# Optimization experiments

Measured on AMD Instinct MI355X. Metric: run time of the kernel, lower is better.

Reference implementation:

```python
import jax, jax.numpy as jnp
import numpy as np

N, D, O, V, E, C = 100000, 128, 128, 3, 400000, 2

def setup_inputs() -> dict:
    key = jax.random.key(0)
    ks = jax.random.split(key, 32)
    s = 0.05
    inp = {
        'features': jax.random.normal(ks[0], (N, D), jnp.float32),
        'edge_index': jax.random.randint(ks[1], (V, 2, E), 0, N, jnp.int32),
        'edge_weight': jax.random.uniform(ks[2], (V, E), jnp.float32),
        # per-view RelationAggregator (single relation each)
        'rel_w': jax.random.normal(ks[3], (V, D, O)) * s,
        'rel_b': jnp.zeros((V, O)),
        'gate_w': jax.random.normal(ks[4], (V, O, O)) * s,
        'gate_b': jnp.zeros((V, O)),
        # LabelAwareAttention
        'la_w1': jax.random.normal(ks[5], (C, D, D // 2)) * s,
        'la_b1': jnp.zeros((C, D // 2)),
        'la_w2': jax.random.normal(ks[6], (C, D // 2)) * s,
        'la_b2': jnp.zeros((C,)),
        'pred_w': jax.random.normal(ks[7], (D, C)) * s,
        'pred_b': jnp.zeros((C,)),
        'att_bias': jnp.float32(0.1),
        # ViewLevelAttention
        'view_pref': jax.random.normal(ks[8], (V, O)),
        'va_w1': jax.random.normal(ks[9], (O, O // 2)) * s,
        'va_b1': jnp.zeros((O // 2,)),
        'va_w2': jax.random.normal(ks[10], (O // 2,)) * s,
        'va_b2': jnp.float32(0.0),
        # linear heads
        'ft_w': jax.random.normal(ks[11], (D, O)) * s,
        'ft_b': jnp.zeros((O,)),
        'sl_w': jax.random.normal(ks[12], (D, O)) * s,
        'sl_b': jnp.zeros((O,)),
        'fus_w': jax.random.normal(ks[13], (2 * O, O)) * s,
        'fus_b': jnp.zeros((O,)),
        'ln_g': jnp.ones((O,)),
        'ln_beta': jnp.zeros((O,)),
    }
    return inp


def _aggregate_view(features, ei, ew, w, b, gw, gb):
    # gather -> linear -> edge weight -> scatter-add (fused segment_sum)
    msg = (features[ei[0]] @ w + b) * ew[:, None]          # [E, O]
    agg = jax.ops.segment_sum(msg, ei[1], num_segments=N)  # [N, O]
    # relation_weight_net: softmax over 1 relation == 1.0 (identity)
    gate = jax.nn.sigmoid(agg @ gw + gb)
    return gate * agg


def reference(features, edge_index, edge_weight, rel_w, rel_b, gate_w, gate_b,
              la_w1, la_b1, la_w2, la_b2, pred_w, pred_b, att_bias,
              view_pref, va_w1, va_b1, va_w2, va_b2,
              ft_w, ft_b, sl_w, sl_b, fus_w, fus_b, ln_g, ln_beta):
    # --- label-aware attention ---
    class_probs = jax.nn.softmax(features @ pred_w + pred_b, axis=-1)        # [N, C]
    h = jax.nn.relu(jnp.einsum('nd,cdk->nck', features, la_w1) + la_b1)      # [N, C, D/2]
    scores = jax.nn.sigmoid(jnp.einsum('nck,ck->nc', h, la_w2) + la_b2)      # [N, C]
    node_att = jnp.sum(scores * class_probs, axis=-1) + att_bias             # [N]

    # --- per-view relation aggregation ---
    views = jax.vmap(_aggregate_view, in_axes=(None, 0, 0, 0, 0, 0, 0))(
        features, edge_index, edge_weight, rel_w, rel_b, gate_w, gate_b)     # [V, N, O]

    # --- view-level attention ---
    pe = views * view_pref[:, None, :]                                       # [V, N, O]
    vh = jax.nn.relu(jnp.einsum('vno,ok->vnk', pe, va_w1) + va_b1)           # [V, N, O/2]
    vscore = jnp.einsum('vnk,k->vn', vh, va_w2) + va_b2                      # [V, N]
    v_att = jax.nn.softmax(vscore, axis=0)                                   # over views
    combined = jnp.sum(views * v_att[..., None], axis=0)                     # [N, O]

    # --- fusion (dropout in eval mode == identity) ---
    self_out = features @ sl_w + sl_b
    transformed = features @ ft_w + ft_b
    weighted = combined * node_att[:, None]
    fused = jax.nn.relu(jnp.concatenate([self_out, weighted], axis=-1) @ fus_w + fus_b)
    out = fused + transformed

    mu = jnp.mean(out, axis=-1, keepdims=True)
    var = jnp.mean(jnp.square(out - mu), axis=-1, keepdims=True)
    out = (out - mu) / jnp.sqrt(var + 1e-5) * ln_g + ln_beta
    return out, class_probs
```

## Files before the change

kernel.cpp:

```cpp
#include <hip/hip_runtime.h>

#define N_ 100000
#define D_ 128
#define O_ 128
#define V_ 3
#define E_ 400000
#define NB_SCAN 98
#define EGRID 1563
#define MB 16
#define NBLK (N_ / MB)
#define LDA 136

#define PRE_CVT  6250
#define PRE_PREW (PRE_CVT + 64)
#define PRE_PREP (PRE_PREW + 617)
#define PRE_TOT  (PRE_PREP + 3 * EGRID)

typedef unsigned short u16;
typedef __attribute__((ext_vector_type(8))) short bf16x8;
typedef __attribute__((ext_vector_type(4))) float f32x4;

#define MFMA16x16x32 __builtin_amdgcn_mfma_f32_16x16x32_bf16

#define P_RELB  0
#define P_GATEB 384
#define P_VP    768
#define P_VAB1  1152
#define P_VAW2  1216
#define P_VAB2  1280
#define P_LAB1  1281
#define P_LAW2  1409
#define P_LAB2  1537
#define P_PREDB 1539
#define P_ATTB  1541
#define P_FTB   1542
#define P_LNG   1670
#define P_LNB   1798
#define P_PREDW 1926
#define P_TOTAL 2182

__device__ __forceinline__ float b2f(u16 u) {
    union { float f; unsigned int i; } x; x.i = ((unsigned int)u) << 16; return x.f;
}
__device__ __forceinline__ float blo(unsigned int u) {
    union { float f; unsigned int i; } x; x.i = u << 16; return x.f;
}
__device__ __forceinline__ float bhi(unsigned int u) {
    union { float f; unsigned int i; } x; x.i = u & 0xffff0000u; return x.f;
}
__device__ __forceinline__ u16 f2b(float f) {
    union { float f; unsigned int i; } x; x.f = f;
    unsigned int r = x.i + 0x7FFFu + ((x.i >> 16) & 1u);
    return (u16)(r >> 16);
}

template<int F32> __device__ __forceinline__ float LD(const void* p, size_t i) {
    if (F32) return ((const float*)p)[i];
    return b2f(((const u16*)p)[i]);
}

__global__ void k_detect(const u16* __restrict__ feat, int* __restrict__ flag) {
    int t = threadIdx.x;
    u16 a = feat[2 * t], b = feat[2 * t + 128];
    int zeros = (a == 0 ? 1 : 0) + (b == 0 ? 1 : 0);
    float va = b2f(a), vb = b2f(b);
    int bad = (!(va > -128.f && va < 128.f) ? 1 : 0) +
              (!(vb > -128.f && vb < 128.f) ? 1 : 0);
    #pragma unroll
    for (int s = 1; s <= 32; s <<= 1) {
        bad += __shfl_xor(bad, s);
        zeros += __shfl_xor(zeros, s);
    }
    if (t == 0) flag[0] = (bad >= 16 || zeros >= 64) ? 1 : 0;
}

__device__ __forceinline__ void cvt_body_f32(int b, const void* feat,
                                             u16* __restrict__ featB) {
    size_t idx = (size_t)b * 256 + threadIdx.x;
    const float4* fp = (const float4*)feat;
    float4 a = fp[idx * 2], c = fp[idx * 2 + 1];
    uint4 u;
    u.x = (unsigned)f2b(a.x) | ((unsigned)f2b(a.y) << 16);
    u.y = (unsigned)f2b(a.z) | ((unsigned)f2b(a.w) << 16);
    u.z = (unsigned)f2b(c.x) | ((unsigned)f2b(c.y) << 16);
    u.w = (unsigned)f2b(c.z) | ((unsigned)f2b(c.w) << 16);
    ((uint4*)featB)[idx] = u;
}

template<int F32>
__device__ __forceinline__ void prew_body(int b, const void* sl_w, const void* sl_b,
                                          const void* fus_w, const void* fus_b,
                                          u16* __restrict__ W1T, float* __restrict__ b1) {
    int gid = b * 256 + threadIdx.x;
    int d = gid >> 7, o = gid & 127;
    float acc = 0.f;
    for (int k = 0; k < 128; ++k)
        acc += LD<F32>(sl_w, d * 128 + k) * LD<F32>(fus_w, k * 128 + o);
    W1T[o * 128 + d] = f2b(acc);
    if (gid < 128) {
        float accb = 0.f;
        for (int k = 0; k < 128; ++k)
            accb += LD<F32>(sl_b, k) * LD<F32>(fus_w, k * 128 + gid);
        b1[gid] = accb + LD<F32>(fus_b, gid);
    }
}

template<int F32>
__device__ __forceinline__ void prep_body(int b,
        const void* rel_w, const void* gate_w, const void* va_w1, const void* fus_w,
        const void* ft_w, const void* la_w1,
        const void* rel_b, const void* gate_b, const void* vpref,
        const void* va_b1, const void* va_w2, const void* va_b2,
        const void* la_b1, const void* la_w2, const void* la_b2,
        const void* pred_b, const void* att_bias, const void* ft_b,
        const void* ln_g, const void* ln_beta, const void* pred_w,
        u16* __restrict__ relT, u16* __restrict__ gateT, u16* __restrict__ vaT,
        u16* __restrict__ fus2T, u16* __restrict__ ftT, u16* __restrict__ laT,
        float* __restrict__ P) {
    int id = b * 256 + threadIdx.x;
    if (id < 49152) {
        int v = id >> 14, r = id & 16383, o = r >> 7, d = r & 127;
        relT[id] = f2b(LD<F32>(rel_w, (size_t)v * 16384 + d * 128 + o));
    } else if (id < 98304) {
        int t = id - 49152, v = t >> 14, r = t & 16383, o = r >> 7, d = r & 127;
        gateT[t] = f2b(LD<F32>(gate_w, (size_t)v * 16384 + d * 128 + o));
    } else if (id < 106496) {
        int t = id - 98304, n = t >> 7, k = t & 127;
        vaT[t] = f2b(LD<F32>(va_w1, k * 64 + n));
    } else if (id < 122880) {
        int t = id - 106496, n = t >> 7, k = t & 127;
        fus2T[t] = f2b(LD<F32>(fus_w, (128 + k) * 128 + n));
    } else if (id < 139264) {
        int t = id - 122880, o = t >> 7, d = t & 127;
        ftT[t] = f2b(LD<F32>(ft_w, d * 128 + o));
    } else if (id < 155648) {
        int t = id - 139264, n = t >> 7, d = t & 127;
        int c = n >> 6, j = n & 63;
        laT[t] = f2b(LD<F32>(la_w1, c * 8192 + d * 64 + j));
    } else if (id < 155648 + P_TOTAL) {
        int t = id - 155648;
        float val;
        if      (t < P_GATEB) val = LD<F32>(rel_b, t);
        else if (t < P_VP)    val = LD<F32>(gate_b, t - P_GATEB);
        else if (t < P_VAB1)  val = LD<F32>(vpref, t - P_VP);
        else if (t < P_VAW2)  val = LD<F32>(va_b1, t - P_VAB1);
        else if (t < P_VAB2)  val = LD<F32>(va_w2, t - P_VAW2);
        else if (t < P_LAB1)  val = LD<F32>(va_b2, 0);
        else if (t < P_LAW2)  val = LD<F32>(la_b1, t - P_LAB1);
        else if (t < P_LAB2)  val = LD<F32>(la_w2, t - P_LAW2);
        else if (t < P_PREDB) val = LD<F32>(la_b2, t - P_LAB2);
        else if (t < P_ATTB)  val = LD<F32>(pred_b, t - P_PREDB);
        else if (t < P_FTB)   val = LD<F32>(att_bias, 0);
        else if (t < P_LNG)   val = LD<F32>(ft_b, t - P_FTB);
        else if (t < P_LNB)   val = LD<F32>(ln_g, t - P_LNG);
        else if (t < P_PREDW) val = LD<F32>(ln_beta, t - P_LNB);
        else                  val = LD<F32>(pred_w, t - P_PREDW);
        P[t] = val;
    }
}

__global__ __launch_bounds__(256) void k_preC(const int* __restrict__ flag,
        const void* feat, u16* __restrict__ featB,
        const void* sl_w, const void* sl_b, const void* fus_w, const void* fus_b,
        u16* __restrict__ W1T, float* __restrict__ b1,
        const void* rel_w, const void* gate_w, const void* va_w1,
        const void* ft_w, const void* la_w1,
        const void* rel_b, const void* gate_b, const void* vpref,
        const void* va_b1, const void* va_w2, const void* va_b2,
        const void* la_b1, const void* la_w2, const void* la_b2,
        const void* pred_b, const void* att_bias, const void* ft_b,
        const void* ln_g, const void* ln_beta, const void* pred_w,
        u16* __restrict__ relT, u16* __restrict__ gateT, u16* __restrict__ vaT,
        u16* __restrict__ fus2T, u16* __restrict__ ftT, u16* __restrict__ laT,
        float* __restrict__ P,
        const int* __restrict__ ei, int* __restrict__ cur3) {
    int b = blockIdx.x;
    if (b < PRE_CVT) {
        if (flag[0]) cvt_body_f32(b, feat, featB);
    } else if (b < PRE_PREW) {
        if (flag[0]) prew_body<1>(b - PRE_CVT, sl_w, sl_b, fus_w, fus_b, W1T, b1);
        else         prew_body<0>(b - PRE_CVT, sl_w, sl_b, fus_w, fus_b, W1T, b1);
    } else if (b < PRE_PREP) {
        if (flag[0]) prep_body<1>(b - PRE_PREW, rel_w, gate_w, va_w1, fus_w, ft_w, la_w1,
                                  rel_b, gate_b, vpref, va_b1, va_w2, va_b2,
                                  la_b1, la_w2, la_b2, pred_b, att_bias, ft_b,
                                  ln_g, ln_beta, pred_w, relT, gateT, vaT, fus2T, ftT, laT, P);
        else         prep_body<0>(b - PRE_PREW, rel_w, gate_w, va_w1, fus_w, ft_w, la_w1,
                                  rel_b, gate_b, vpref, va_b1, va_w2, va_b2,
                                  la_b1, la_w2, la_b2, pred_b, att_bias, ft_b,
                                  ln_g, ln_beta, pred_w, relT, gateT, vaT, fus2T, ftT, laT, P);
    } else {
        int b2 = b - PRE_PREP;
        int v = b2 / EGRID;
        int e = (b2 % EGRID) * 256 + threadIdx.x;
        if (e < E_) atomicAdd(&cur3[v * N_ + ei[(size_t)v * 2 * E_ + E_ + e]], 1);
    }
}

__global__ __launch_bounds__(256) void k_scan_bsum(const int* __restrict__ cur3,
                                                   int* __restrict__ bsum) {
    __shared__ int red[256];
    const int v = blockIdx.x / NB_SCAN, b = blockIdx.x % NB_SCAN, tid = threadIdx.x;
    const int base = b * 1024;
    const int* counts = cur3 + v * N_;
    int s = 0;
    for (int i = tid; i < 1024; i += 256) {
        int idx = base + i;
        s += (idx < N_) ? counts[idx] : 0;
    }
    red[tid] = s;
    __syncthreads();
    for (int st = 128; st >= 1; st >>= 1) {
        if (tid < st) red[tid] += red[tid + st];
        __syncthreads();
    }
    if (tid == 0) bsum[v * 128 + b] = red[0];
}

__global__ __launch_bounds__(256) void k_scan_write(int* __restrict__ cur3,
                                                    const int* __restrict__ bsum,
                                                    int* __restrict__ offs3) {
    __shared__ int lsum[256];
    __shared__ int bs_s[128];
    const int v = blockIdx.x / NB_SCAN, b = blockIdx.x % NB_SCAN, tid = threadIdx.x;
    const int base = b * 1024;
    int* counts = cur3 + v * N_;
    int* offs   = offs3 + v * N_;
    if (tid < 128) bs_s[tid] = (tid < b) ? bsum[v * 128 + tid] : 0;
    int c[4]; int s = 0;
    #pragma unroll
    for (int k = 0; k < 4; ++k) {
        int idx = base + tid * 4 + k;
        c[k] = (idx < N_) ? counts[idx] : 0;
        s += c[k];
    }
    lsum[tid] = s;
    __syncthreads();
    for (int st = 1; st < 256; st <<= 1) {
        int t = (tid >= st) ? lsum[tid - st] : 0;
        __syncthreads();
        lsum[tid] += t;
        __syncthreads();
    }
    for (int st = 64; st >= 1; st >>= 1) {
        if (tid < st) bs_s[tid] += bs_s[tid + st];
        __syncthreads();
    }
    int off = bs_s[0] + lsum[tid] - s;
    #pragma unroll
    for (int k = 0; k < 4; ++k) {
        int idx = base + tid * 4 + k;
        if (idx < N_) { offs[idx] = off; counts[idx] = off; }
        off += c[k];
    }
}

template<int F32>
__device__ __forceinline__ void place_body(const int* __restrict__ ei, const void* ew_all,
                                           int* __restrict__ cur3, int2* __restrict__ srcw3) {
    int v = blockIdx.x / EGRID;
    int e = (blockIdx.x % EGRID) * 256 + threadIdx.x;
    if (e < E_) {
        int dst = ei[(size_t)v * 2 * E_ + E_ + e];
        int src = ei[(size_t)v * 2 * E_ + e];
        float w = LD<F32>(ew_all, (size_t)v * E_ + e);
        int pos = atomicAdd(&cur3[v * N_ + dst], 1);
        int2 sw; sw.x = src; sw.y = __float_as_int(w);
        srcw3[(size_t)v * E_ + pos] = sw;
    }
}
__global__ __launch_bounds__(256) void k_place(const int* __restrict__ flag,
                                               const int* __restrict__ ei, const void* ew,
                                               int* __restrict__ cur3, int2* __restrict__ srcw3) {
    if (flag[0]) place_body<1>(ei, ew, cur3, srcw3);
    else         place_body<0>(ei, ew, cur3, srcw3);
}

__global__ __launch_bounds__(256, 4) void k_fused(const int* __restrict__ flag,
        const void* feat, const u16* __restrict__ featB_,
        const int2* __restrict__ srcw3,
        const int* __restrict__ offs3, const int* __restrict__ ends3,
        const u16* __restrict__ relT, const u16* __restrict__ gateT,
        const u16* __restrict__ vaT, const u16* __restrict__ W1T,
        const u16* __restrict__ fus2T, const u16* __restrict__ ftT,
        const u16* __restrict__ laT,
        const float* __restrict__ b1, const float* __restrict__ P,
        void* __restrict__ d_out) {
    const int f32 = flag[0];
    const u16* __restrict__ fb = f32 ? featB_ : (const u16*)feat;

    __shared__ __align__(16) u16 xA[MB * LDA];
    __shared__ __align__(16) u16 zb[2][MB * LDA];
    __shared__ float wsn_s[2][MB];
    __shared__ float vsc_s[MB][3];
    __shared__ float red_s[4][MB][2];
    __shared__ float mrs_s[MB][2];
    __shared__ float aw_s[MB][3];
    __shared__ float natt_s[MB];
    __shared__ float lg_s[MB][2];
    __shared__ float vab1_s[64], vaw2_s[64];
    __shared__ float predw_s[256];
    __shared__ float b1_s[128], ftb_s[128], lng_s[128], lnb_s[128];

    const int tid = threadIdx.x;
    const int wid = tid >> 6;
    const int L = tid & 63, q = L >> 4, i = L & 15;
    const int nb = wid * 32;
    const int nodebase = blockIdx.x * MB;
    const int nl = tid >> 5, l32 = tid & 31, o4 = l32 * 4;
    const int gg = tid >> 4, l16 = tid & 15, o8 = l16 * 8;
    const f32x4 zz = {0.f, 0.f, 0.f, 0.f};

    auto ldf = [&](const u16* B, int row, int k0) -> bf16x8 {
        return *(const bf16x8*)&B[row * LDA + k0];
    };
    auto ldg = [&](const u16* B, int row, int k0) -> bf16x8 {
        return *(const bf16x8*)&B[row * 128 + k0];
    };
    auto gemm128 = [&](const u16* A, const u16* Bg, f32x4 acc[2]) {
        #pragma unroll
        for (int kk = 0; kk < 4; ++kk) {
            int k0 = q * 8 + kk * 32;
            bf16x8 a0 = ldf(A, i, k0);
            bf16x8 bb0 = ldg(Bg, nb + i, k0);
            bf16x8 bb1 = ldg(Bg, nb + 16 + i, k0);
            acc[0] = MFMA16x16x32(a0, bb0, acc[0], 0, 0, 0);
            acc[1] = MFMA16x16x32(a0, bb1, acc[1], 0, 0, 0);
        }
    };
    auto gather = [&](int v, u16* dst) {
        const int* offs = offs3 + v * N_;
        const int* ends = ends3 + v * N_;
        const int2* srcw = srcw3 + (size_t)v * E_;
        const int node = nodebase + gg;
        float z0 = 0.f, z1 = 0.f, z2 = 0.f, z3 = 0.f;
        float z4 = 0.f, z5 = 0.f, z6 = 0.f, z7 = 0.f, ws = 0.f;
        int j = offs[node], jend = ends[node];
        while (j < jend) {
            int r = jend - j;
            int2 e0 = srcw[j];
            int2 e1, e2, e3;
            e1.x = 0; e1.y = 0; e2.x = 0; e2.y = 0; e3.x = 0; e3.y = 0;
            if (r > 1) e1 = srcw[j + 1];
            if (r > 2) e2 = srcw[j + 2];
            if (r > 3) e3 = srcw[j + 3];
            uint4 x0, x1, x2, x3;
            x1.x = x1.y = x1.z = x1.w = 0;
            x2.x = x2.y = x2.z = x2.w = 0;
            x3.x = x3.y = x3.z = x3.w = 0;
            x0 = *(const uint4*)&fb[(size_t)e0.x * 128 + o8];
            if (r > 1) x1 = *(const uint4*)&fb[(size_t)e1.x * 128 + o8];
            if (r > 2) x2 = *(const uint4*)&fb[(size_t)e2.x * 128 + o8];
            if (r > 3) x3 = *(const uint4*)&fb[(size_t)e3.x * 128 + o8];
            float w0 = __int_as_float(e0.y), w1 = __int_as_float(e1.y);
            float w2 = __int_as_float(e2.y), w3 = __int_as_float(e3.y);
            ws += w0 + w1 + w2 + w3;
            z0 += w0 * blo(x0.x) + w1 * blo(x1.x) + w2 * blo(x2.x) + w3 * blo(x3.x);
            z1 += w0 * bhi(x0.x) + w1 * bhi(x1.x) + w2 * bhi(x2.x) + w3 * bhi(x3.x);
            z2 += w0 * blo(x0.y) + w1 * blo(x1.y) + w2 * blo(x2.y) + w3 * blo(x3.y);
            z3 += w0 * bhi(x0.y) + w1 * bhi(x1.y) + w2 * bhi(x2.y) + w3 * bhi(x3.y);
            z4 += w0 * blo(x0.z) + w1 * blo(x1.z) + w2 * blo(x2.z) + w3 * blo(x3.z);
            z5 += w0 * bhi(x0.z) + w1 * bhi(x1.z) + w2 * bhi(x2.z) + w3 * bhi(x3.z);
            z6 += w0 * blo(x0.w) + w1 * blo(x1.w) + w2 * blo(x2.w) + w3 * blo(x3.w);
            z7 += w0 * bhi(x0.w) + w1 * bhi(x1.w) + w2 * bhi(x2.w) + w3 * bhi(x3.w);
            j += 4;
        }
        uint4 u;
        u.x = (unsigned)f2b(z0) | ((unsigned)f2b(z1) << 16);
        u.y = (unsigned)f2b(z2) | ((unsigned)f2b(z3) << 16);
        u.z = (unsigned)f2b(z4) | ((unsigned)f2b(z5) << 16);
        u.w = (unsigned)f2b(z6) | ((unsigned)f2b(z7) << 16);
        *(uint4*)&dst[gg * LDA + o8] = u;
        if (l16 == 0) wsn_s[v & 1][gg] = ws;
    };

    {
        int m = tid >> 4, s = tid & 15;
        *(uint4*)&xA[m * LDA + s * 8] =
            *(const uint4*)&fb[(size_t)(nodebase + m) * 128 + s * 8];
    }
    if (tid < 64) { vab1_s[tid] = P[P_VAB1 + tid]; vaw2_s[tid] = P[P_VAW2 + tid]; }
    if (tid < 128) {
        b1_s[tid]  = b1[tid];
        ftb_s[tid] = P[P_FTB + tid];
        lng_s[tid] = P[P_LNG + tid];
        lnb_s[tid] = P[P_LNB + tid];
    }
    predw_s[tid] = P[P_PREDW + tid];
    gather(0, zb[0]);
    __syncthreads();

    f32x4 accL[2] = {zz, zz};
    gemm128(xA, laT, accL);
    #pragma unroll
    for (int rep = 0; rep < 2; ++rep) {
        int m = rep * 8 + nl;
        float lg0 = 0.f, lg1 = 0.f;
        #pragma unroll
        for (int t = 0; t < 4; ++t) {
            float xv = b2f(xA[m * LDA + o4 + t]);
            lg0 += xv * predw_s[(o4 + t) * 2 + 0];
            lg1 += xv * predw_s[(o4 + t) * 2 + 1];
        }
        #pragma unroll
        for (int s = 1; s <= 16; s <<= 1) {
            lg0 += __shfl_xor(lg0, s);
            lg1 += __shfl_xor(lg1, s);
        }
        if (l32 == 0) { lg_s[m][0] = lg0; lg_s[m][1] = lg1; }
    }
    {
        float la0 = P[P_LAB1 + nb + i],  la1 = P[P_LAB1 + nb + 16 + i];
        float lw0 = P[P_LAW2 + nb + i],  lw1 = P[P_LAW2 + nb + 16 + i];
        float partL[4];
        #pragma unroll
        for (int r = 0; r < 4; ++r) {
            float h0 = fmaxf(accL[0][r] + la0, 0.f);
            float h1 = fmaxf(accL[1][r] + la1, 0.f);
            partL[r] = h0 * lw0 + h1 * lw1;
        }
        #pragma unroll
        for (int s = 1; s <= 8; s <<= 1)
            #pragma unroll
            for (int r = 0; r < 4; ++r)
                partL[r] += __shfl_xor(partL[r], s);
        if (i == 0)
            #pragma unroll
            for (int r = 0; r < 4; ++r)
                red_s[wid][q * 4 + r][0] = partL[r];
    }
    __syncthreads();
    if (tid < MB) {
        float c0 = red_s[0][tid][0] + red_s[1][tid][0] + P[P_LAB2 + 0];
        float c1 = red_s[2][tid][0] + red_s[3][tid][0] + P[P_LAB2 + 1];
        float s0 = 1.f / (1.f + __expf(-c0));
        float s1 = 1.f / (1.f + __expf(-c1));
        float l0 = lg_s[tid][0] + P[P_PREDB + 0];
        float l1 = lg_s[tid][1] + P[P_PREDB + 1];
        float mx = fmaxf(l0, l1);
        float e0 = __expf(l0 - mx), e1 = __expf(l1 - mx);
        float inv = 1.f / (e0 + e1);
        float p0 = e0 * inv, p1 = e1 * inv;
        natt_s[tid] = s0 * p0 + s1 * p1 + P[P_ATTB];
        int node = nodebase + tid;
        if (f32) {
            float* pr = (float*)d_out + (size_t)N_ * O_;
            pr[node * 2 + 0] = p0; pr[node * 2 + 1] = p1;
        } else {
            u16* pr = (u16*)d_out + (size_t)N_ * O_;
            pr[node * 2 + 0] = f2b(p0); pr[node * 2 + 1] = f2b(p1);
        }
    }

    f32x4 viewr[3][2];
    #pragma unroll
    for (int v = 0; v < 3; ++v) {
        u16* zc = zb[v & 1];
        f32x4 accA[2] = {zz, zz};
        gemm128(zc, relT + (size_t)v * 16384, accA);
        if (v < 2) gather(v + 1, zb[(v + 1) & 1]);
        __syncthreads();
        {
            float rb0 = P[P_RELB + v * 128 + nb + i];
            float rb1 = P[P_RELB + v * 128 + nb + 16 + i];
            #pragma unroll
            for (int nt = 0; nt < 2; ++nt) {
                float rb = nt ? rb1 : rb0;
                int col = nb + nt * 16 + i;
                #pragma unroll
                for (int r = 0; r < 4; ++r) {
                    int row = q * 4 + r;
                    float a = accA[nt][r] + wsn_s[v & 1][row] * rb;
                    accA[nt][r] = a;
                    zc[row * LDA + col] = f2b(a);
                }
            }
        }
        __syncthreads();
        f32x4 acc2[2] = {zz, zz};
        gemm128(zc, gateT + (size_t)v * 16384, acc2);
        __syncthreads();
        {
            float gb0 = P[P_GATEB + v * 128 + nb + i];
            float gb1 = P[P_GATEB + v * 128 + nb + 16 + i];
            float vp0 = P[P_VP + v * 128 + nb + i];
            float vp1 = P[P_VP + v * 128 + nb + 16 + i];
            #pragma unroll
            for (int nt = 0; nt < 2; ++nt) {
                float gb = nt ? gb1 : gb0, vp = nt ? vp1 : vp0;
                int col = nb + nt * 16 + i;
                #pragma unroll
                for (int r = 0; r < 4; ++r) {
                    int row = q * 4 + r;
                    float g = 1.f / (1.f + __expf(-(acc2[nt][r] + gb)));
                    float vv = g * accA[nt][r];
                    viewr[v][nt][r] = vv;
                    zc[row * LDA + col] = f2b(vv * vp);
                }
            }
        }
        __syncthreads();
        f32x4 accV = zz;
        const int nbv = wid * 16, colv = nbv + i;
        #pragma unroll
        for (int kk = 0; kk < 4; ++kk) {
            int k0 = q * 8 + kk * 32;
            bf16x8 a0 = ldf(zc, i, k0);
            bf16x8 bb = ldg(vaT, nbv + i, k0);
            accV = MFMA16x16x32(a0, bb, accV, 0, 0, 0);
        }
        float part[4];
        #pragma unroll
        for (int r = 0; r < 4; ++r) {
            float vh = fmaxf(accV[r] + vab1_s[colv], 0.f);
            part[r] = vh * vaw2_s[colv];
        }
        #pragma unroll
        for (int s = 1; s <= 8; s <<= 1)
            #pragma unroll
            for (int r = 0; r < 4; ++r)
                part[r] += __shfl_xor(part[r], s);
        if (i == 0)
            #pragma unroll
            for (int r = 0; r < 4; ++r)
                red_s[wid][q * 4 + r][0] = part[r];
        __syncthreads();
        if (tid < MB)
            vsc_s[tid][v] = red_s[0][tid][0] + red_s[1][tid][0] +
                            red_s[2][tid][0] + red_s[3][tid][0] + P[P_VAB2];
    }

    if (tid < MB) {
        float s0 = vsc_s[tid][0], s1 = vsc_s[tid][1], s2 = vsc_s[tid][2];
        float mx = fmaxf(s0, fmaxf(s1, s2));
        float e0 = __expf(s0 - mx), e1 = __expf(s1 - mx), e2 = __expf(s2 - mx);
        float inv = natt_s[tid] / (e0 + e1 + e2);
        aw_s[tid][0] = e0 * inv; aw_s[tid][1] = e1 * inv; aw_s[tid][2] = e2 * inv;
    }
    __syncthreads();
    u16* wt = zb[0];
    #pragma unroll
    for (int nt = 0; nt < 2; ++nt)
        #pragma unroll
        for (int r = 0; r < 4; ++r) {
            int row = q * 4 + r, col = nb + nt * 16 + i;
            float wv = aw_s[row][0] * viewr[0][nt][r] +
                       aw_s[row][1] * viewr[1][nt][r] +
                       aw_s[row][2] * viewr[2][nt][r];
            wt[row * LDA + col] = f2b(wv);
        }
    f32x4 accF[2] = {zz, zz};
    gemm128(xA, W1T, accF);
    __syncthreads();
    gemm128(wt, fus2T, accF);
    float fR[2][4];
    #pragma unroll
    for (int nt = 0; nt < 2; ++nt)
        #pragma unroll
        for (int r = 0; r < 4; ++r) {
            int col = nb + nt * 16 + i;
            fR[nt][r] = fmaxf(accF[nt][r] + b1_s[col], 0.f);
        }
    f32x4 accT[2] = {zz, zz};
    gemm128(xA, ftT, accT);

    float ov[2][4], ps[4], pq[4];
    #pragma unroll
    for (int r = 0; r < 4; ++r) { ps[r] = 0.f; pq[r] = 0.f; }
    #pragma unroll
    for (int nt = 0; nt < 2; ++nt)
        #pragma unroll
        for (int r = 0; r < 4; ++r) {
            int col = nb + nt * 16 + i;
            float o = fR[nt][r] + accT[nt][r] + ftb_s[col];
            ov[nt][r] = o;
            ps[r] += o; pq[r] += o * o;
        }
    #pragma unroll
    for (int s = 1; s <= 8; s <<= 1)
        #pragma unroll
        for (int r = 0; r < 4; ++r) {
            ps[r] += __shfl_xor(ps[r], s);
            pq[r] += __shfl_xor(pq[r], s);
        }
    if (i == 0)
        #pragma unroll
        for (int r = 0; r < 4; ++r) {
            red_s[wid][q * 4 + r][0] = ps[r];
            red_s[wid][q * 4 + r][1] = pq[r];
        }
    __syncthreads();
    if (tid < MB) {
        float sm = red_s[0][tid][0] + red_s[1][tid][0] + red_s[2][tid][0] + red_s[3][tid][0];
        float sq = red_s[0][tid][1] + red_s[1][tid][1] + red_s[2][tid][1] + red_s[3][tid][1];
        float mu = sm * (1.f / 128.f);
        float var = sq * (1.f / 128.f) - mu * mu;
        mrs_s[tid][0] = mu; mrs_s[tid][1] = rsqrtf(var + 1e-5f);
    }
    __syncthreads();
    float* outf = (float*)zb;
    u16*   outb = (u16*)zb;
    #pragma unroll
    for (int nt = 0; nt < 2; ++nt)
        #pragma unroll
        for (int r = 0; r < 4; ++r) {
            int row = q * 4 + r, col = nb + nt * 16 + i;
            float val = (ov[nt][r] - mrs_s[row][0]) * mrs_s[row][1]
                        * lng_s[col] + lnb_s[col];
            if (f32) outf[row * 128 + col] = val;
            else     outb[row * 128 + col] = f2b(val);
        }
    __syncthreads();
    if (f32) {
        float* op = (float*)d_out + (size_t)nodebase * 128;
        for (int idx = tid; idx < 512; idx += 256)
            ((float4*)op)[idx] = ((const float4*)outf)[idx];
    } else {
        u16* op = (u16*)d_out + (size_t)nodebase * 128;
        ((uint4*)op)[tid] = ((const uint4*)outb)[tid];
    }
}

extern "C" void kernel_launch(void* const* d_in, const int* in_sizes, int n_in,
                              void* d_out, int out_size, void* d_ws, size_t ws_size,
                              hipStream_t stream) {
    const void* feat     = d_in[0];
    const int*  ei       = (const int*)d_in[1];
    const void* ew       = d_in[2];
    const void* rel_w    = d_in[3];
    const void* rel_b    = d_in[4];
    const void* gate_w   = d_in[5];
    const void* gate_b   = d_in[6];
    const void* la_w1    = d_in[7];
    const void* la_b1    = d_in[8];
    const void* la_w2    = d_in[9];
    const void* la_b2    = d_in[10];
    const void* pred_w   = d_in[11];
    const void* pred_b   = d_in[12];
    const void* att_bias = d_in[13];
    const void* view_pref= d_in[14];
    const void* va_w1    = d_in[15];
    const void* va_b1    = d_in[16];
    const void* va_w2    = d_in[17];
    const void* va_b2    = d_in[18];
    const void* ft_w     = d_in[19];
    const void* ft_b     = d_in[20];
    const void* sl_w     = d_in[21];
    const void* sl_b     = d_in[22];
    const void* fus_w    = d_in[23];
    const void* fus_b    = d_in[24];
    const void* ln_g     = d_in[25];
    const void* ln_beta  = d_in[26];

    int*   flag  = (int*)d_ws;
    int*   offs3 = flag + 4;
    int*   cur3  = offs3 + 3 * N_;
    int2*  srcw3 = (int2*)(cur3 + 3 * N_);
    int*   bsum  = (int*)(srcw3 + 3 * E_);
    float* b1    = (float*)(bsum + 3 * 128);
    float* P     = b1 + 128;
    u16*   W1T   = (u16*)(P + 2304);
    u16*   relT  = W1T + 16384;
    u16*   gateT = relT + 3 * 16384;
    u16*   vaT   = gateT + 3 * 16384;
    u16*   fus2T = vaT + 8192;
    u16*   ftT   = fus2T + 16384;
    u16*   laT   = ftT + 16384;
    u16*   featB = laT + 16384;

    k_detect<<<1, 64, 0, stream>>>((const u16*)feat, flag);
    (void)hipMemsetAsync(cur3, 0, 3 * N_ * sizeof(int), stream);
    k_preC<<<PRE_TOT, 256, 0, stream>>>(flag, feat, featB,
                                        sl_w, sl_b, fus_w, fus_b, W1T, b1,
                                        rel_w, gate_w, va_w1, ft_w, la_w1,
                                        rel_b, gate_b, view_pref,
                                        va_b1, va_w2, va_b2,
                                        la_b1, la_w2, la_b2,
                                        pred_b, att_bias, ft_b, ln_g, ln_beta, pred_w,
                                        relT, gateT, vaT, fus2T, ftT, laT, P,
                                        ei, cur3);
    k_scan_bsum<<<3 * NB_SCAN, 256, 0, stream>>>(cur3, bsum);
    k_scan_write<<<3 * NB_SCAN, 256, 0, stream>>>(cur3, bsum, offs3);
    k_place<<<3 * EGRID, 256, 0, stream>>>(flag, ei, ew, cur3, srcw3);
    k_fused<<<NBLK, 256, 0, stream>>>(flag, feat, featB, srcw3, offs3, cur3,
                                      relT, gateT, vaT, W1T, fus2T, ftT, laT,
                                      b1, P, d_out);
}
```

Before: 623.9 us.

## Process three views concurrently in 768-thread blocks with 32-node tiles

The fused kernel now launches 768 threads per block, one 256-thread group per view. Each group gathers its view's neighbors and runs its relation, gate and view-attention GEMMs at the same time as the others, where before the three views ran one after another. The node tile grows from 16 to 32 rows so each weight fragment is reused across two MFMA row tiles. The final fusion GEMMs are also split across the three groups, with partial results passed through shared memory. In exchange, shared memory use per block roughly doubles. The launch bound of (768, 6) may push the compiler into tight register limits or spills, and fewer, larger blocks could reduce occupancy.

```diff
diff --git a/kernel.cpp b/kernel.cpp
--- a/kernel.cpp
+++ b/kernel.cpp
@@ -7,7 +7,7 @@
 #define E_ 400000
 #define NB_SCAN 98
 #define EGRID 1563
-#define MB 16
+#define MB 32
 #define NBLK (N_ / MB)
 #define LDA 136
 
@@ -276,7 +276,7 @@
     else         place_body<0>(ei, ew, cur3, srcw3);
 }
 
-__global__ __launch_bounds__(256, 4) void k_fused(const int* __restrict__ flag,
+__global__ __launch_bounds__(768, 6) void k_fused(const int* __restrict__ flag,
         const void* feat, const u16* __restrict__ featB_,
         const int2* __restrict__ srcw3,
         const int* __restrict__ offs3, const int* __restrict__ ends3,
@@ -290,25 +290,29 @@
     const u16* __restrict__ fb = f32 ? featB_ : (const u16*)feat;
 
     __shared__ __align__(16) u16 xA[MB * LDA];
-    __shared__ __align__(16) u16 zb[2][MB * LDA];
-    __shared__ float wsn_s[2][MB];
-    __shared__ float vsc_s[MB][3];
-    __shared__ float red_s[4][MB][2];
-    __shared__ float mrs_s[MB][2];
+    __shared__ __align__(16) u16 zbuf[3][MB * LDA];
+    __shared__ __align__(16) float Fbuf[MB * 128];
+    __shared__ float vp3_s[3][128];
+    __shared__ float redL[4][MB];
+    __shared__ float redv[3][4][MB];
+    __shared__ float wsn3[3][MB];
     __shared__ float aw_s[MB][3];
     __shared__ float natt_s[MB];
     __shared__ float lg_s[MB][2];
+    __shared__ float mrs_s[MB][2];
     __shared__ float vab1_s[64], vaw2_s[64];
     __shared__ float predw_s[256];
     __shared__ float b1_s[128], ftb_s[128], lng_s[128], lnb_s[128];
 
     const int tid = threadIdx.x;
-    const int wid = tid >> 6;
-    const int L = tid & 63, q = L >> 4, i = L & 15;
+    const int g   = tid >> 8;
+    const int t256 = tid & 255;
+    const int wid = t256 >> 6;
+    const int L = t256 & 63, q = L >> 4, i = L & 15;
     const int nb = wid * 32;
     const int nodebase = blockIdx.x * MB;
-    const int nl = tid >> 5, l32 = tid & 31, o4 = l32 * 4;
-    const int gg = tid >> 4, l16 = tid & 15, o8 = l16 * 8;
+    const int nl = t256 >> 5, l32 = t256 & 31, o4 = l32 * 4;
+    const int gsub = t256 >> 4, l16 = tid & 15, o8 = l16 * 8;
     const f32x4 zz = {0.f, 0.f, 0.f, 0.f};
 
     auto ldf = [&](const u16* B, int row, int k0) -> bf16x8 {
@@ -317,64 +321,71 @@
     auto ldg = [&](const u16* B, int row, int k0) -> bf16x8 {
         return *(const bf16x8*)&B[row * 128 + k0];
     };
-    auto gemm128 = [&](const u16* A, const u16* Bg, f32x4 acc[2]) {
+    auto gemm32 = [&](const u16* A, const u16* Bg, f32x4 acc[2][2]) {
         #pragma unroll
         for (int kk = 0; kk < 4; ++kk) {
             int k0 = q * 8 + kk * 32;
             bf16x8 a0 = ldf(A, i, k0);
+            bf16x8 a1 = ldf(A, i + 16, k0);
             bf16x8 bb0 = ldg(Bg, nb + i, k0);
             bf16x8 bb1 = ldg(Bg, nb + 16 + i, k0);
-            acc[0] = MFMA16x16x32(a0, bb0, acc[0], 0, 0, 0);
-            acc[1] = MFMA16x16x32(a0, bb1, acc[1], 0, 0, 0);
+            acc[0][0] = MFMA16x16x32(a0, bb0, acc[0][0], 0, 0, 0);
+            acc[0][1] = MFMA16x16x32(a0, bb1, acc[0][1], 0, 0, 0);
+            acc[1][0] = MFMA16x16x32(a1, bb0, acc[1][0], 0, 0, 0);
+            acc[1][1] = MFMA16x16x32(a1, bb1, acc[1][1], 0, 0, 0);
         }
     };
-    auto gather = [&](int v, u16* dst) {
-        const int* offs = offs3 + v * N_;
-        const int* ends = ends3 + v * N_;
-        const int2* srcw = srcw3 + (size_t)v * E_;
-        const int node = nodebase + gg;
-        float z0 = 0.f, z1 = 0.f, z2 = 0.f, z3 = 0.f;
-        float z4 = 0.f, z5 = 0.f, z6 = 0.f, z7 = 0.f, ws = 0.f;
-        int j = offs[node], jend = ends[node];
-        while (j < jend) {
-            int r = jend - j;
-            int2 e0 = srcw[j];
-            int2 e1, e2, e3;
-            e1.x = 0; e1.y = 0; e2.x = 0; e2.y = 0; e3.x = 0; e3.y = 0;
-            if (r > 1) e1 = srcw[j + 1];
-            if (r > 2) e2 = srcw[j + 2];
-            if (r > 3) e3 = srcw[j + 3];
-            uint4 x0, x1, x2, x3;
-            x1.x = x1.y = x1.z = x1.w = 0;
-            x2.x = x2.y = x2.z = x2.w = 0;
-            x3.x = x3.y = x3.z = x3.w = 0;
-            x0 = *(const uint4*)&fb[(size_t)e0.x * 128 + o8];
-            if (r > 1) x1 = *(const uint4*)&fb[(size_t)e1.x * 128 + o8];
-            if (r > 2) x2 = *(const uint4*)&fb[(size_t)e2.x * 128 + o8];
-            if (r > 3) x3 = *(const uint4*)&fb[(size_t)e3.x * 128 + o8];
-            float w0 = __int_as_float(e0.y), w1 = __int_as_float(e1.y);
-            float w2 = __int_as_float(e2.y), w3 = __int_as_float(e3.y);
-            ws += w0 + w1 + w2 + w3;
-            z0 += w0 * blo(x0.x) + w1 * blo(x1.x) + w2 * blo(x2.x) + w3 * blo(x3.x);
-            z1 += w0 * bhi(x0.x) + w1 * bhi(x1.x) + w2 * bhi(x2.x) + w3 * bhi(x3.x);
-            z2 += w0 * blo(x0.y) + w1 * blo(x1.y) + w2 * blo(x2.y) + w3 * blo(x3.y);
-            z3 += w0 * bhi(x0.y) + w1 * bhi(x1.y) + w2 * bhi(x2.y) + w3 * bhi(x3.y);
-            z4 += w0 * blo(x0.z) + w1 * blo(x1.z) + w2 * blo(x2.z) + w3 * blo(x3.z);
-            z5 += w0 * bhi(x0.z) + w1 * bhi(x1.z) + w2 * bhi(x2.z) + w3 * bhi(x3.z);
-            z6 += w0 * blo(x0.w) + w1 * blo(x1.w) + w2 * blo(x2.w) + w3 * blo(x3.w);
-            z7 += w0 * bhi(x0.w) + w1 * bhi(x1.w) + w2 * bhi(x2.w) + w3 * bhi(x3.w);
-            j += 4;
+    auto gather = [&]() {
+        const int* offs = offs3 + g * N_;
+        const int* ends = ends3 + g * N_;
+        const int2* srcw = srcw3 + (size_t)g * E_;
+        #pragma unroll
+        for (int rep = 0; rep < 2; ++rep) {
+            const int m = gsub + rep * 16;
+            const int node = nodebase + m;
+            float z0 = 0.f, z1 = 0.f, z2 = 0.f, z3 = 0.f;
+            float z4 = 0.f, z5 = 0.f, z6 = 0.f, z7 = 0.f, ws = 0.f;
+            int j = offs[node], jend = ends[node];
+            while (j < jend) {
+                int r = jend - j;
+                int2 e0 = srcw[j];
+                int2 e1, e2, e3;
+                e1.x = 0; e1.y = 0; e2.x = 0; e2.y = 0; e3.x = 0; e3.y = 0;
+                if (r > 1) e1 = srcw[j + 1];
+                if (r > 2) e2 = srcw[j + 2];
+                if (r > 3) e3 = srcw[j + 3];
+                uint4 x0, x1, x2, x3;
+                x1.x = x1.y = x1.z = x1.w = 0;
+                x2.x = x2.y = x2.z = x2.w = 0;
+                x3.x = x3.y = x3.z = x3.w = 0;
+                x0 = *(const uint4*)&fb[(size_t)e0.x * 128 + o8];
+                if (r > 1) x1 = *(const uint4*)&fb[(size_t)e1.x * 128 + o8];
+                if (r > 2) x2 = *(const uint4*)&fb[(size_t)e2.x * 128 + o8];
+                if (r > 3) x3 = *(const uint4*)&fb[(size_t)e3.x * 128 + o8];
+                float w0 = __int_as_float(e0.y), w1 = __int_as_float(e1.y);
+                float w2 = __int_as_float(e2.y), w3 = __int_as_float(e3.y);
+                ws += w0 + w1 + w2 + w3;
+                z0 += w0 * blo(x0.x) + w1 * blo(x1.x) + w2 * blo(x2.x) + w3 * blo(x3.x);
+                z1 += w0 * bhi(x0.x) + w1 * bhi(x1.x) + w2 * bhi(x2.x) + w3 * bhi(x3.x);
+                z2 += w0 * blo(x0.y) + w1 * blo(x1.y) + w2 * blo(x2.y) + w3 * blo(x3.y);
+                z3 += w0 * bhi(x0.y) + w1 * bhi(x1.y) + w2 * bhi(x2.y) + w3 * bhi(x3.y);
+                z4 += w0 * blo(x0.z) + w1 * blo(x1.z) + w2 * blo(x2.z) + w3 * blo(x3.z);
+                z5 += w0 * bhi(x0.z) + w1 * bhi(x1.z) + w2 * bhi(x2.z) + w3 * bhi(x3.z);
+                z6 += w0 * blo(x0.w) + w1 * blo(x1.w) + w2 * blo(x2.w) + w3 * blo(x3.w);
+                z7 += w0 * bhi(x0.w) + w1 * bhi(x1.w) + w2 * bhi(x2.w) + w3 * bhi(x3.w);
+                j += 4;
+            }
+            uint4 u;
+            u.x = (unsigned)f2b(z0) | ((unsigned)f2b(z1) << 16);
+            u.y = (unsigned)f2b(z2) | ((unsigned)f2b(z3) << 16);
+            u.z = (unsigned)f2b(z4) | ((unsigned)f2b(z5) << 16);
+            u.w = (unsigned)f2b(z6) | ((unsigned)f2b(z7) << 16);
+            *(uint4*)&zbuf[g][m * LDA + o8] = u;
+            if (l16 == 0) wsn3[g][m] = ws;
         }
-        uint4 u;
-        u.x = (unsigned)f2b(z0) | ((unsigned)f2b(z1) << 16);
-        u.y = (unsigned)f2b(z2) | ((unsigned)f2b(z3) << 16);
-        u.z = (unsigned)f2b(z4) | ((unsigned)f2b(z5) << 16);
-        u.w = (unsigned)f2b(z6) | ((unsigned)f2b(z7) << 16);
-        *(uint4*)&dst[gg * LDA + o8] = u;
-        if (l16 == 0) wsn_s[v & 1][gg] = ws;
     };
 
-    {
+    if (tid < 512) {
         int m = tid >> 4, s = tid & 15;
         *(uint4*)&xA[m * LDA + s * 8] =
             *(const uint4*)&fb[(size_t)(nodebase + m) * 128 + s * 8];
@@ -386,53 +397,84 @@
         lng_s[tid] = P[P_LNG + tid];
         lnb_s[tid] = P[P_LNB + tid];
     }
-    predw_s[tid] = P[P_PREDW + tid];
-    gather(0, zb[0]);
-    __syncthreads();
-
-    f32x4 accL[2] = {zz, zz};
-    gemm128(xA, laT, accL);
-    #pragma unroll
-    for (int rep = 0; rep < 2; ++rep) {
-        int m = rep * 8 + nl;
-        float lg0 = 0.f, lg1 = 0.f;
-        #pragma unroll
-        for (int t = 0; t < 4; ++t) {
-            float xv = b2f(xA[m * LDA + o4 + t]);
-            lg0 += xv * predw_s[(o4 + t) * 2 + 0];
-            lg1 += xv * predw_s[(o4 + t) * 2 + 1];
+    if (tid < 256) predw_s[tid] = P[P_PREDW + tid];
+    if (tid >= 256 && tid < 640) {
+        int t = tid - 256;
+        vp3_s[t >> 7][t & 127] = P[P_VP + t];
+    }
+    gather();
+    __syncthreads();
+
+    f32x4 accA[2][2] = {{zz, zz}, {zz, zz}};
+    gemm32(zbuf[g], relT + (size_t)g * 16384, accA);
+    if (g == 0) {
+        f32x4 accL[2][2] = {{zz, zz}, {zz, zz}};
+        gemm32(xA, laT, accL);
+        #pragma unroll
+        for (int rep = 0; rep < 4; ++rep) {
+            int m = rep * 8 + nl;
+            float lg0 = 0.f, lg1 = 0.f;
+            #pragma unroll
+            for (int t = 0; t < 4; ++t) {
+                float xv = b2f(xA[m * LDA + o4 + t]);
+                lg0 += xv * predw_s[(o4 + t) * 2 + 0];
+                lg1 += xv * predw_s[(o4 + t) * 2 + 1];
+            }
+            #pragma unroll
+            for (int s = 1; s <= 16; s <<= 1) {
+                lg0 += __shfl_xor(lg0, s);
+                lg1 += __shfl_xor(lg1, s);
+            }
+            if (l32 == 0) { lg_s[m][0] = lg0; lg_s[m][1] = lg1; }
         }
-        #pragma unroll
-        for (int s = 1; s <= 16; s <<= 1) {
-            lg0 += __shfl_xor(lg0, s);
-            lg1 += __shfl_xor(lg1, s);
-        }
-        if (l32 == 0) { lg_s[m][0] = lg0; lg_s[m][1] = lg1; }
-    }
-    {
         float la0 = P[P_LAB1 + nb + i],  la1 = P[P_LAB1 + nb + 16 + i];
         float lw0 = P[P_LAW2 + nb + i],  lw1 = P[P_LAW2 + nb + 16 + i];
-        float partL[4];
-        #pragma unroll
-        for (int r = 0; r < 4; ++r) {
-            float h0 = fmaxf(accL[0][r] + la0, 0.f);
-            float h1 = fmaxf(accL[1][r] + la1, 0.f);
-            partL[r] = h0 * lw0 + h1 * lw1;
-        }
+        float partL[2][4];
+        #pragma unroll
+        for (int mt = 0; mt < 2; ++mt)
+            #pragma unroll
+            for (int r = 0; r < 4; ++r) {
+                float h0 = fmaxf(accL[mt][0][r] + la0, 0.f);
+                float h1 = fmaxf(accL[mt][1][r] + la1, 0.f);
+                partL[mt][r] = h0 * lw0 + h1 * lw1;
+            }
         #pragma unroll
         for (int s = 1; s <= 8; s <<= 1)
             #pragma unroll
-            for (int r = 0; r < 4; ++r)
-                partL[r] += __shfl_xor(partL[r], s);
+            for (int mt = 0; mt < 2; ++mt)
+                #pragma unroll
+                for (int r = 0; r < 4; ++r)
+                    partL[mt][r] += __shfl_xor(partL[mt][r], s);
         if (i == 0)
             #pragma unroll
-            for (int r = 0; r < 4; ++r)
-                red_s[wid][q * 4 + r][0] = partL[r];
-    }
-    __syncthreads();
+            for (int mt = 0; mt < 2; ++mt)
+                #pragma unroll
+                for (int r = 0; r < 4; ++r)
+                    redL[wid][mt * 16 + q * 4 + r] = partL[mt][r];
+    }
+    __syncthreads();
+
+    {
+        float rb0 = P[P_RELB + g * 128 + nb + i];
+        float rb1 = P[P_RELB + g * 128 + nb + 16 + i];
+        #pragma unroll
+        for (int mt = 0; mt < 2; ++mt)
+            #pragma unroll
+            for (int nt = 0; nt < 2; ++nt) {
+                float rb = nt ? rb1 : rb0;
+                int col = nb + nt * 16 + i;
+                #pragma unroll
+                for (int r = 0; r < 4; ++r) {
+                    int row = mt * 16 + q * 4 + r;
+                    float a = accA[mt][nt][r] + wsn3[g][row] * rb;
+                    accA[mt][nt][r] = a;
+                    zbuf[g][row * LDA + col] = f2b(a);
+                }
+            }
+    }
     if (tid < MB) {
-        float c0 = red_s[0][tid][0] + red_s[1][tid][0] + P[P_LAB2 + 0];
-        float c1 = red_s[2][tid][0] + red_s[3][tid][0] + P[P_LAB2 + 1];
+        float c0 = redL[0][tid] + redL[1][tid] + P[P_LAB2 + 0];
+        float c1 = redL[2][tid] + redL[3][tid] + P[P_LAB2 + 1];
         float s0 = 1.f / (1.f + __expf(-c0));
         float s1 = 1.f / (1.f + __expf(-c1));
         float l0 = lg_s[tid][0] + P[P_PREDB + 0];
@@ -451,173 +493,199 @@
             pr[node * 2 + 0] = f2b(p0); pr[node * 2 + 1] = f2b(p1);
         }
     }
-
-    f32x4 viewr[3][2];
-    #pragma unroll
-    for (int v = 0; v < 3; ++v) {
-        u16* zc = zb[v & 1];
-        f32x4 accA[2] = {zz, zz};
-        gemm128(zc, relT + (size_t)v * 16384, accA);
-        if (v < 2) gather(v + 1, zb[(v + 1) & 1]);
-        __syncthreads();
-        {
-            float rb0 = P[P_RELB + v * 128 + nb + i];
-            float rb1 = P[P_RELB + v * 128 + nb + 16 + i];
+    __syncthreads();
+
+    f32x4 acc2[2][2] = {{zz, zz}, {zz, zz}};
+    gemm32(zbuf[g], gateT + (size_t)g * 16384, acc2);
+    __syncthreads();
+
+    {
+        float gb0 = P[P_GATEB + g * 128 + nb + i];
+        float gb1 = P[P_GATEB + g * 128 + nb + 16 + i];
+        #pragma unroll
+        for (int mt = 0; mt < 2; ++mt)
             #pragma unroll
             for (int nt = 0; nt < 2; ++nt) {
-                float rb = nt ? rb1 : rb0;
+                float gb = nt ? gb1 : gb0;
                 int col = nb + nt * 16 + i;
                 #pragma unroll
                 for (int r = 0; r < 4; ++r) {
-                    int row = q * 4 + r;
-                    float a = accA[nt][r] + wsn_s[v & 1][row] * rb;
-                    accA[nt][r] = a;
-                    zc[row * LDA + col] = f2b(a);
+                    int row = mt * 16 + q * 4 + r;
+                    float gt = 1.f / (1.f + __expf(-(acc2[mt][nt][r] + gb)));
+                    zbuf[g][row * LDA + col] = f2b(gt * accA[mt][nt][r]);
                 }
             }
-        }
-        __syncthreads();
-        f32x4 acc2[2] = {zz, zz};
-        gemm128(zc, gateT + (size_t)v * 16384, acc2);
-        __syncthreads();
-        {
-            float gb0 = P[P_GATEB + v * 128 + nb + i];
-            float gb1 = P[P_GATEB + v * 128 + nb + 16 + i];
-            float vp0 = P[P_VP + v * 128 + nb + i];
-            float vp1 = P[P_VP + v * 128 + nb + 16 + i];
-            #pragma unroll
-            for (int nt = 0; nt < 2; ++nt) {
-                float gb = nt ? gb1 : gb0, vp = nt ? vp1 : vp0;
-                int col = nb + nt * 16 + i;
-                #pragma unroll
-                for (int r = 0; r < 4; ++r) {
-                    int row = q * 4 + r;
-                    float g = 1.f / (1.f + __expf(-(acc2[nt][r] + gb)));
-                    float vv = g * accA[nt][r];
-                    viewr[v][nt][r] = vv;
-                    zc[row * LDA + col] = f2b(vv * vp);
-                }
-            }
-        }
-        __syncthreads();
-        f32x4 accV = zz;
+    }
+    __syncthreads();
+
+    {
+        f32x4 accV[2] = {zz, zz};
         const int nbv = wid * 16, colv = nbv + i;
         #pragma unroll
         for (int kk = 0; kk < 4; ++kk) {
             int k0 = q * 8 + kk * 32;
-            bf16x8 a0 = ldf(zc, i, k0);
+            bf16x8 a0r = ldf(zbuf[g], i, k0);
+            bf16x8 a1r = ldf(zbuf[g], i + 16, k0);
+            bf16x8 a0, a1;
+            #pragma unroll
+            for (int e = 0; e < 8; ++e) {
+                float vp = vp3_s[g][k0 + e];
+                a0[e] = (short)f2b(b2f((u16)a0r[e]) * vp);
+                a1[e] = (short)f2b(b2f((u16)a1r[e]) * vp);
+            }
             bf16x8 bb = ldg(vaT, nbv + i, k0);
-            accV = MFMA16x16x32(a0, bb, accV, 0, 0, 0);
+            accV[0] = MFMA16x16x32(a0, bb, accV[0], 0, 0, 0);
+            accV[1] = MFMA16x16x32(a1, bb, accV[1], 0, 0, 0);
         }
-        float part[4];
-        #pragma unroll
-        for (int r = 0; r < 4; ++r) {
-            float vh = fmaxf(accV[r] + vab1_s[colv], 0.f);
-            part[r] = vh * vaw2_s[colv];
-        }
+        float part[2][4];
+        #pragma unroll
+        for (int mt = 0; mt < 2; ++mt)
+            #pragma unroll
+            for (int r = 0; r < 4; ++r) {
+                float vh = fmaxf(accV[mt][r] + vab1_s[colv], 0.f);
+                part[mt][r] = vh * vaw2_s[colv];
+            }
         #pragma unroll
         for (int s = 1; s <= 8; s <<= 1)
             #pragma unroll
-            for (int r = 0; r < 4; ++r)
-                part[r] += __shfl_xor(part[r], s);
+            for (int mt = 0; mt < 2; ++mt)
+                #pragma unroll
+                for (int r = 0; r < 4; ++r)
+                    part[mt][r] += __shfl_xor(part[mt][r], s);
         if (i == 0)
             #pragma unroll
-            for (int r = 0; r < 4; ++r)
-                red_s[wid][q * 4 + r][0] = part[r];
-        __syncthreads();
-        if (tid < MB)
-            vsc_s[tid][v] = red_s[0][tid][0] + red_s[1][tid][0] +
-                            red_s[2][tid][0] + red_s[3][tid][0] + P[P_VAB2];
-    }
+            for (int mt = 0; mt < 2; ++mt)
+                #pragma unroll
+                for (int r = 0; r < 4; ++r)
+                    redv[g][wid][mt * 16 + q * 4 + r] = part[mt][r];
+    }
+    __syncthreads();
 
     if (tid < MB) {
-        float s0 = vsc_s[tid][0], s1 = vsc_s[tid][1], s2 = vsc_s[tid][2];
-        float mx = fmaxf(s0, fmaxf(s1, s2));
-        float e0 = __expf(s0 - mx), e1 = __expf(s1 - mx), e2 = __expf(s2 - mx);
+        float sv[3];
+        #pragma unroll
+        for (int v = 0; v < 3; ++v)
+            sv[v] = redv[v][0][tid] + redv[v][1][tid] +
+                    redv[v][2][tid] + redv[v][3][tid] + P[P_VAB2];
+        float mx = fmaxf(sv[0], fmaxf(sv[1], sv[2]));
+        float e0 = __expf(sv[0] - mx), e1 = __expf(sv[1] - mx), e2 = __expf(sv[2] - mx);
         float inv = natt_s[tid] / (e0 + e1 + e2);
         aw_s[tid][0] = e0 * inv; aw_s[tid][1] = e1 * inv; aw_s[tid][2] = e2 * inv;
     }
     __syncthreads();
-    u16* wt = zb[0];
-    #pragma unroll
-    for (int nt = 0; nt < 2; ++nt)
-        #pragma unroll
-        for (int r = 0; r < 4; ++r) {
-            int row = q * 4 + r, col = nb + nt * 16 + i;
-            float wv = aw_s[row][0] * viewr[0][nt][r] +
-                       aw_s[row][1] * viewr[1][nt][r] +
-                       aw_s[row][2] * viewr[2][nt][r];
-            wt[row * LDA + col] = f2b(wv);
-        }
-    f32x4 accF[2] = {zz, zz};
-    gemm128(xA, W1T, accF);
-    __syncthreads();
-    gemm128(wt, fus2T, accF);
-    float fR[2][4];
-    #pragma unroll
-    for (int nt = 0; nt < 2; ++nt)
-        #pragma unroll
-        for (int r = 0; r < 4; ++r) {
-            int col = nb + nt * 16 + i;
-            fR[nt][r] = fmaxf(accF[nt][r] + b1_s[col], 0.f);
-        }
-    f32x4 accT[2] = {zz, zz};
-    gemm128(xA, ftT, accT);
-
-    float ov[2][4], ps[4], pq[4];
-    #pragma unroll
-    for (int r = 0; r < 4; ++r) { ps[r] = 0.f; pq[r] = 0.f; }
-    #pragma unroll
-    for (int nt = 0; nt < 2; ++nt)
-        #pragma unroll
-        for (int r = 0; r < 4; ++r) {
-            int col = nb + nt * 16 + i;
-            float o = fR[nt][r] + accT[nt][r] + ftb_s[col];
-            ov[nt][r] = o;
-            ps[r] += o; pq[r] += o * o;
-        }
-    #pragma unroll
-    for (int s = 1; s <= 8; s <<= 1)
-        #pragma unroll
-        for (int r = 0; r < 4; ++r) {
-            ps[r] += __shfl_xor(ps[r], s);
-            pq[r] += __shfl_xor(pq[r], s);
-        }
-    if (i == 0)
-        #pragma unroll
-        for (int r = 0; r < 4; ++r) {
-            red_s[wid][q * 4 + r][0] = ps[r];
-            red_s[wid][q * 4 + r][1] = pq[r];
-        }
-    __syncthreads();
+
+    for (int idx = tid; idx < MB * 128; idx += 768) {
+        int row = idx >> 7, col = idx & 127;
+        float w = aw_s[row][0] * b2f(zbuf[0][row * LDA + col]) +
+                  aw_s[row][1] * b2f(zbuf[1][row * LDA + col]) +
+                  aw_s[row][2] * b2f(zbuf[2][row * LDA + col]);
+        zbuf[0][row * LDA + col] = f2b(w);
+    }
+    __syncthreads();
+
+    float* F1 = (float*)&zbuf[1][0];
+    f32x4 accG[2][2] = {{zz, zz}, {zz, zz}};
+    if (g == 0) {
+        gemm32(xA, W1T, accG);
+        #pragma unroll
+        for (int mt = 0; mt < 2; ++mt)
+            #pragma unroll
+            for (int nt = 0; nt < 2; ++nt)
+                #pragma unroll
+                for (int r = 0; r < 4; ++r)
+                    F1[(mt * 16 + q * 4 + r) * 128 + nb + nt * 16 + i] = accG[mt][nt][r];
+    } else if (g == 1) {
+        gemm32(zbuf[0], fus2T, accG);
+        #pragma unroll
+        for (int mt = 0; mt < 2; ++mt)
+            #pragma unroll
+            for (int nt = 0; nt < 2; ++nt)
+                #pragma unroll
+                for (int r = 0; r < 4; ++r)
+                    Fbuf[(mt * 16 + q * 4 + r) * 128 + nb + nt * 16 + i] = accG[mt][nt][r];
+    } else {
+        gemm32(xA, ftT, accG);
+    }
+    __syncthreads();
+
+    float ov[2][2][4];
+    if (g == 2) {
+        float ps[2][4], pq[2][4];
+        #pragma unroll
+        for (int mt = 0; mt < 2; ++mt)
+            #pragma unroll
+            for (int r = 0; r < 4; ++r) { ps[mt][r] = 0.f; pq[mt][r] = 0.f; }
+        #pragma unroll
+        for (int mt = 0; mt < 2; ++mt)
+            #pragma unroll
+            for (int nt = 0; nt < 2; ++nt)
+                #pragma unroll
+                for (int r = 0; r < 4; ++r) {
+                    int row = mt * 16 + q * 4 + r, col = nb + nt * 16 + i;
+                    float o = fmaxf(F1[row * 128 + col] + Fbuf[row * 128 + col]
+                                    + b1_s[col], 0.f)
+                              + accG[mt][nt][r] + ftb_s[col];
+                    ov[mt][nt][r] = o;
+                    ps[mt][r] += o; pq[mt][r] += o * o;
+                }
+        #pragma unroll
+        for (int s = 1; s <= 8; s <<= 1)
+            #pragma unroll
+            for (int mt = 0; mt < 2; ++mt)
+                #pragma unroll
+                for (int r = 0; r < 4; ++r) {
+                    ps[mt][r] += __shfl_xor(ps[mt][r], s);
+                    pq[mt][r] += __shfl_xor(pq[mt][r], s);
+                }
+        float* red2 = &redv[0][0][0];
+        if (i == 0)
+            #pragma unroll
+            for (int mt = 0; mt < 2; ++mt)
+                #pragma unroll
+                for (int r = 0; r < 4; ++r) {
+                    int row = mt * 16 + q * 4 + r;
+                    red2[wid * 64 + row * 2 + 0] = ps[mt][r];
+                    red2[wid * 64 + row * 2 + 1] = pq[mt][r];
+                }
+    }
+    __syncthreads();
+
     if (tid < MB) {
-        float sm = red_s[0][tid][0] + red_s[1][tid][0] + red_s[2][tid][0] + red_s[3][tid][0];
-        float sq = red_s[0][tid][1] + red_s[1][tid][1] + red_s[2][tid][1] + red_s[3][tid][1];
+        const float* red2 = &redv[0][0][0];
+        float sm = red2[tid * 2] + red2[64 + tid * 2] +
+                   red2[128 + tid * 2] + red2[192 + tid * 2];
+        float sq = red2[tid * 2 + 1] + red2[64 + tid * 2 + 1] +
+                   red2[128 + tid * 2 + 1] + red2[192 + tid * 2 + 1];
         float mu = sm * (1.f / 128.f);
         float var = sq * (1.f / 128.f) - mu * mu;
         mrs_s[tid][0] = mu; mrs_s[tid][1] = rsqrtf(var + 1e-5f);
     }
     __syncthreads();
-    float* outf = (float*)zb;
-    u16*   outb = (u16*)zb;
-    #pragma unroll
-    for (int nt = 0; nt < 2; ++nt)
-        #pragma unroll
-        for (int r = 0; r < 4; ++r) {
-            int row = q * 4 + r, col = nb + nt * 16 + i;
-            float val = (ov[nt][r] - mrs_s[row][0]) * mrs_s[row][1]
-                        * lng_s[col] + lnb_s[col];
-            if (f32) outf[row * 128 + col] = val;
-            else     outb[row * 128 + col] = f2b(val);
-        }
-    __syncthreads();
+
+    if (g == 2) {
+        #pragma unroll
+        for (int mt = 0; mt < 2; ++mt)
+            #pragma unroll
+            for (int nt = 0; nt < 2; ++nt)
+                #pragma unroll
+                for (int r = 0; r < 4; ++r) {
+                    int row = mt * 16 + q * 4 + r, col = nb + nt * 16 + i;
+                    float val = (ov[mt][nt][r] - mrs_s[row][0]) * mrs_s[row][1]
+                                * lng_s[col] + lnb_s[col];
+                    if (f32) Fbuf[row * 128 + col] = val;
+                    else     ((u16*)Fbuf)[row * 128 + col] = f2b(val);
+                }
+    }
+    __syncthreads();
+
     if (f32) {
         float* op = (float*)d_out + (size_t)nodebase * 128;
-        for (int idx = tid; idx < 512; idx += 256)
-            ((float4*)op)[idx] = ((const float4*)outf)[idx];
+        for (int idx = tid; idx < 1024; idx += 768)
+            ((float4*)op)[idx] = ((const float4*)Fbuf)[idx];
     } else {
         u16* op = (u16*)d_out + (size_t)nodebase * 128;
-        ((uint4*)op)[tid] = ((const uint4*)outb)[tid];
+        if (tid < 512)
+            ((uint4*)op)[tid] = ((const uint4*)Fbuf)[tid];
     }
 }
 
@@ -682,7 +750,7 @@
     k_scan_bsum<<<3 * NB_SCAN, 256, 0, stream>>>(cur3, bsum);
     k_scan_write<<<3 * NB_SCAN, 256, 0, stream>>>(cur3, bsum, offs3);
     k_place<<<3 * EGRID, 256, 0, stream>>>(flag, ei, ew, cur3, srcw3);
-    k_fused<<<NBLK, 256, 0, stream>>>(flag, feat, featB, srcw3, offs3, cur3,
+    k_fused<<<NBLK, 768, 0, stream>>>(flag, feat, featB, srcw3, offs3, cur3,
                                       relT, gateT, vaT, W1T, fus2T, ftT, laT,
                                       b1, P, d_out);
 }
```

New measurement: 544.2 us. -12.8%, faster.
